# Kernel tuning notes

Hardware: AMD Instinct MI355X
Metric: run time of the kernel (lower is better)

The kernel has to match this reference:

```python
import jax, jax.numpy as jnp
import numpy as np

NUM_KP = 34
NUM_CP = 10
DEGREE = 3
NUM_KNOTS = NUM_CP + DEGREE + 1  # 14
B = 32768


def _lin(k, i, o):
    return jax.random.normal(k, (i, o), jnp.float32) * (1.0 / np.sqrt(i))


def setup_inputs() -> dict:
    key = jax.random.key(0)
    ks = jax.random.split(key, 18)
    keypoints = jax.random.normal(ks[0], (B, NUM_KP, 2), jnp.float32)
    # clamped cubic base knot vector: [0]*4 + 6 interior + [1]*4
    interior = jnp.linspace(0.0, 1.0, 8)[1:-1]
    base = jnp.concatenate([jnp.zeros(4), interior, jnp.ones(4)]).astype(jnp.float32)
    knots = jnp.tile(base[None, :], (B, 1))
    cp = jax.random.normal(ks[1], (B, NUM_CP, 2), jnp.float32)
    return {
        'keypoints': keypoints, 'knots': knots, 'cp': cp,
        'w1': _lin(ks[2], NUM_KP * 2, 256), 'b1': jnp.zeros(256, jnp.float32),
        'w2': _lin(ks[3], 256, 512), 'b2': jnp.zeros(512, jnp.float32),
        'w3': _lin(ks[4], 512, 256), 'b3': jnp.zeros(256, jnp.float32),
        'wc1': _lin(ks[5], 256, 128), 'bc1': jnp.zeros(128, jnp.float32),
        'wc2': _lin(ks[6], 128, NUM_CP * 2), 'bc2': jnp.zeros(NUM_CP * 2, jnp.float32),
        'wk1': _lin(ks[7], 256, 128), 'bk1': jnp.zeros(128, jnp.float32),
        'wk2': _lin(ks[8], 128, NUM_KNOTS - 8), 'bk2': jnp.zeros(NUM_KNOTS - 8, jnp.float32),
    }


def bspline_points(u, cpts, uq):
    """Cox-de Boor evaluation. u: (14,), cpts: (10,2), uq: (Q,). Returns (Q,2)."""
    uq = jnp.minimum(uq, u[-1] - 1e-6)  # handle u=1 endpoint of clamped knots
    # degree-0 basis: (Q, 13)
    N = ((uq[:, None] >= u[None, :-1]) & (uq[:, None] < u[None, 1:])).astype(cpts.dtype)
    for p in range(1, DEGREE + 1):
        left_den = u[p:-1] - u[:-p - 1]
        right_den = u[p + 1:] - u[1:-p]
        left = jnp.where(left_den > 0, (uq[:, None] - u[None, :-p - 1]) / left_den, 0.0)
        right = jnp.where(right_den > 0, (u[None, p + 1:] - uq[:, None]) / right_den, 0.0)
        N = left * N[:, :-1] + right * N[:, 1:]
    return N @ cpts  # (Q,10)@(10,2)


def cobb_line(pts):
    """Cobb angles (PT, MT, TL) in degrees from curve points (34,2)."""
    d = pts[1:] - pts[:-1]  # (33,2) tangents
    ang = jnp.degrees(jnp.arctan2(d[:, 0], d[:, 1]))  # tilt w.r.t. vertical axis
    i_max = jnp.argmax(ang)
    i_min = jnp.argmin(ang)
    mt = ang[i_max] - ang[i_min]
    lo = jnp.minimum(i_max, i_min)
    hi = jnp.maximum(i_max, i_min)
    idx = jnp.arange(ang.shape[0])
    up = jnp.where(idx <= lo, ang, ang[lo])
    pt = jnp.max(up) - jnp.min(up)
    dn = jnp.where(idx >= hi, ang, ang[hi])
    tl = jnp.max(dn) - jnp.min(dn)
    return jnp.stack([pt, mt, tl])


def reference(keypoints, knots, cp, w1, b1, w2, b2, w3, b3,
              wc1, bc1, wc2, bc2, wk1, bk1, wk2, bk2):
    bsz = keypoints.shape[0]
    x = keypoints.reshape(bsz, -1)  # [B, 68]
    # feature extractor (eval mode: dropout = identity)
    h = jax.nn.relu(x @ w1 + b1)
    h = jax.nn.relu(h @ w2 + b2)
    feat = jax.nn.relu(h @ w3 + b3)  # [B, 256]
    # control-point head
    cp_flat = jax.nn.relu(feat @ wc1 + bc1) @ wc2 + bc2
    deta_cp = cp_flat.reshape(bsz, NUM_CP, 2)
    cps = deta_cp + cp
    # knot head with Hardtanh(0,1)
    deta_knots_6 = jnp.clip(jax.nn.relu(feat @ wk1 + bk1) @ wk2 + bk2, 0.0, 1.0)
    zeros4 = jnp.zeros((bsz, 4), deta_knots_6.dtype)
    knots_full = jnp.concatenate([zeros4, deta_knots_6, zeros4], axis=1) + knots
    # batched de-Boor spline eval + Cobb geometry (replaces per-sample loop)
    uq = jnp.linspace(0.0, 1.0, NUM_KP).astype(jnp.float32)
    pts = jax.vmap(lambda u, c: bspline_points(u, c, uq))(knots_full, cps)  # [B,34,2]
    cobb_angles = jax.vmap(cobb_line)(pts)  # [B,3]
    return cobb_angles, deta_cp, deta_knots_6
```

## Files before the change

### kernel.cpp

```cpp
#include <hip/hip_runtime.h>
#include <math.h>

#define BLOCK 256
#define MS 16


__device__ __forceinline__ void unpack16(const float* __restrict__ row, float* av){
  const float4* r4 = (const float4*)row;
  float4 a0=r4[0], a1=r4[1], a2=r4[2], a3=r4[3];
  av[0]=a0.x;  av[1]=a0.y;  av[2]=a0.z;  av[3]=a0.w;
  av[4]=a1.x;  av[5]=a1.y;  av[6]=a1.z;  av[7]=a1.w;
  av[8]=a2.x;  av[9]=a2.y;  av[10]=a2.z; av[11]=a2.w;
  av[12]=a3.x; av[13]=a3.y; av[14]=a3.z; av[15]=a3.w;
}

template<int K, int N, int VEC, bool RELU>
__device__ __forceinline__ void dense_layer(const float* __restrict__ W,
                                            const float* __restrict__ Bv,
                                            const float* sA, float* sC, int tid)
{
  static_assert(N == BLOCK*VEC, "each thread owns VEC consecutive columns");
  const int j0 = tid*VEC;
  float acc[VEC][MS];
  #pragma unroll
  for (int c=0;c<VEC;c++){
    float b = Bv[j0+c];
    #pragma unroll
    for (int m=0;m<MS;m++) acc[c][m] = b;
  }
  #pragma unroll 4
  for (int k=0;k<K;k++){
    float av[MS];
    unpack16(sA + k*MS, av);
    float w[VEC];
    if constexpr (VEC == 2){
      float2 wv = *(const float2*)(W + (size_t)k*N + j0);
      w[0]=wv.x; w[1]=wv.y;
    } else {
      w[0] = W[(size_t)k*N + j0];
    }
    #pragma unroll
    for (int c=0;c<VEC;c++){
      #pragma unroll
      for (int m=0;m<MS;m++) acc[c][m] = fmaf(av[m], w[c], acc[c][m]);
    }
  }
  #pragma unroll
  for (int c=0;c<VEC;c++){
    #pragma unroll
    for (int m=0;m<MS;m++){
      float v = acc[c][m];
      if (RELU) v = fmaxf(v, 0.f);
      sC[(size_t)(j0+c)*MS + m] = v;
    }
  }
}

extern "C" __global__ __launch_bounds__(BLOCK, 3)
void kbs_mlp(const float* __restrict__ kp,
             const float* __restrict__ w1, const float* __restrict__ b1,
             const float* __restrict__ w2, const float* __restrict__ b2,
             const float* __restrict__ w3, const float* __restrict__ b3,
             const float* __restrict__ wc1, const float* __restrict__ bc1,
             const float* __restrict__ wc2, const float* __restrict__ bc2,
             const float* __restrict__ wk1, const float* __restrict__ bk1,
             const float* __restrict__ wk2, const float* __restrict__ bk2,
             float* __restrict__ dout, int B)
{
  __shared__ float sA[512*MS];
  __shared__ float sB[256*MS];

  const int tid = threadIdx.x;
  const long base = (long)blockIdx.x * MS;

  for (int idx = tid; idx < 68*MS; idx += BLOCK){
    int m = idx / 68, k = idx % 68;
    float v = 0.f;
    if (base + m < B) v = kp[(base + m)*68 + k];
    sA[k*MS + m] = v;
  }
  __syncthreads();

  dense_layer<68, 256, 1, true>(w1, b1, sA, sB, tid);
  __syncthreads();
  dense_layer<256,512, 2, true>(w2, b2, sB, sA, tid);
  __syncthreads();
  dense_layer<512,256, 1, true>(w3, b3, sA, sB, tid);
  __syncthreads();

  float* sHC = sA;
  float* sHK = sA + 128*MS;
  {
    const bool isC = (tid < 128);
    const int j = tid & 127;
    const float* W  = isC ? wc1 : wk1;
    const float* Bv = isC ? bc1 : bk1;
    float acc[MS];
    float b = Bv[j];
    #pragma unroll
    for (int m=0;m<MS;m++) acc[m] = b;
    #pragma unroll 4
    for (int k=0;k<256;k++){
      float av[MS];
      unpack16(sB + k*MS, av);
      float w = W[k*128 + j];
      #pragma unroll
      for (int m=0;m<MS;m++) acc[m] = fmaf(av[m], w, acc[m]);
    }
    float* dst = isC ? sHC : sHK;
    #pragma unroll
    for (int m=0;m<MS;m++) dst[j*MS + m] = fmaxf(acc[m], 0.f);
  }
  __syncthreads();

  float* sCPF = sB;
  float* sK6  = sB + 20*MS;
  if (tid < 20){
    float acc[MS];
    float b = bc2[tid];
    #pragma unroll
    for (int m=0;m<MS;m++) acc[m] = b;
    for (int k=0;k<128;k++){
      float av[MS];
      unpack16(sHC + k*MS, av);
      float w = wc2[k*20 + tid];
      #pragma unroll
      for (int m=0;m<MS;m++) acc[m] = fmaf(av[m], w, acc[m]);
    }
    #pragma unroll
    for (int m=0;m<MS;m++) sCPF[tid*MS + m] = acc[m];
  } else if (tid >= 64 && tid < 70){
    const int j = tid - 64;
    float acc[MS];
    float b = bk2[j];
    #pragma unroll
    for (int m=0;m<MS;m++) acc[m] = b;
    for (int k=0;k<128;k++){
      float av[MS];
      unpack16(sHK + k*MS, av);
      float w = wk2[k*6 + j];
      #pragma unroll
      for (int m=0;m<MS;m++) acc[m] = fmaf(av[m], w, acc[m]);
    }
    #pragma unroll
    for (int m=0;m<MS;m++) sK6[j*MS + m] = fminf(fmaxf(acc[m], 0.f), 1.f);
  }
  __syncthreads();

  float* out_dcp = dout + (long)B*3;
  float* out_dk  = dout + (long)B*23;
  for (int idx = tid; idx < MS*20; idx += BLOCK){
    int s = idx / 20, c = idx % 20;
    if (base + s < B) out_dcp[(base+s)*20 + c] = sCPF[c*MS + s];
  }
  for (int idx = tid; idx < MS*6; idx += BLOCK){
    int s = idx / 6, c = idx % 6;
    if (base + s < B) out_dk[(base+s)*6 + c] = sK6[c*MS + s];
  }
}

extern "C" __global__ __launch_bounds__(256)
void kbs_geom(const float* __restrict__ knots_g, const float* __restrict__ cp_g,
              float* __restrict__ dout, int B)
{
  const int s = blockIdx.x * blockDim.x + threadIdx.x;
  if (s >= B) return;

  const float* dcp = dout + (long)B*3  + (long)s*20;
  const float* dk6 = dout + (long)B*23 + (long)s*6;

  double u[14];
  #pragma unroll
  for (int i=0;i<14;i++){
    double d = (i>=4 && i<10) ? (double)dk6[i-4] : 0.0;
    u[i] = (double)knots_g[(long)s*14 + i] + d;
  }
  double cx[10], cy[10];
  #pragma unroll
  for (int i=0;i<10;i++){
    cx[i] = (double)cp_g[(long)s*20 + 2*i    ] + (double)dcp[2*i    ];
    cy[i] = (double)cp_g[(long)s*20 + 2*i + 1] + (double)dcp[2*i + 1];
  }

  double ang[33];
  double ppx = 0.0, ppy = 0.0;
  const double uend = u[13] - 1e-6;
  for (int q = 0; q < 34; ++q){
    double uq = (double)q * (1.0/33.0);
    if (uq > uend) uq = uend;
    double Nb[13];
    #pragma unroll
    for (int i=0;i<13;i++)
      Nb[i] = (uq >= u[i] && uq < u[i+1]) ? 1.0 : 0.0;
    #pragma unroll
    for (int p=1;p<=3;p++){
      #pragma unroll
      for (int i=0;i+p<13;i++){
        double ld = u[i+p]   - u[i];
        double rd = u[i+p+1] - u[i+1];
        double lf = (ld > 0.0) ? (uq - u[i])     / ld : 0.0;
        double rf = (rd > 0.0) ? (u[i+p+1] - uq) / rd : 0.0;
        Nb[i] = lf*Nb[i] + rf*Nb[i+1];
      }
    }
    double px = 0.0, py = 0.0;
    #pragma unroll
    for (int i=0;i<10;i++){ px += Nb[i]*cx[i]; py += Nb[i]*cy[i]; }
    if (q > 0)
      ang[q-1] = 57.29577951308232087679815 * atan2(px - ppx, py - ppy);
    ppx = px; ppy = py;
  }

  int imax = 0, imin = 0;
  for (int i=1;i<33;i++){
    if (ang[i] > ang[imax]) imax = i;
    if (ang[i] < ang[imin]) imin = i;
  }
  double mt = ang[imax] - ang[imin];
  int lo = imax < imin ? imax : imin;
  int hi = imax > imin ? imax : imin;

  double uM = -1e300, um = 1e300;
  for (int i=0;i<=lo;i++){ uM = fmax(uM, ang[i]); um = fmin(um, ang[i]); }
  double dM = -1e300, dm = 1e300;
  for (int i=hi;i<33;i++){ dM = fmax(dM, ang[i]); dm = fmin(dm, ang[i]); }

  dout[(long)s*3 + 0] = (float)(uM - um);
  dout[(long)s*3 + 1] = (float)mt;
  dout[(long)s*3 + 2] = (float)(dM - dm);
}

extern "C" void kernel_launch(void* const* d_in, const int* in_sizes, int n_in,
                              void* d_out, int out_size, void* d_ws, size_t ws_size,
                              hipStream_t stream)
{
  const float* kp    = (const float*)d_in[0];
  const float* knots = (const float*)d_in[1];
  const float* cp    = (const float*)d_in[2];
  const float* w1  = (const float*)d_in[3];  const float* b1  = (const float*)d_in[4];
  const float* w2  = (const float*)d_in[5];  const float* b2  = (const float*)d_in[6];
  const float* w3  = (const float*)d_in[7];  const float* b3  = (const float*)d_in[8];
  const float* wc1 = (const float*)d_in[9];  const float* bc1 = (const float*)d_in[10];
  const float* wc2 = (const float*)d_in[11]; const float* bc2 = (const float*)d_in[12];
  const float* wk1 = (const float*)d_in[13]; const float* bk1 = (const float*)d_in[14];
  const float* wk2 = (const float*)d_in[15]; const float* bk2 = (const float*)d_in[16];

  const int B = in_sizes[0] / 68;
  const int nblkA = (B + MS - 1) / MS;
  const int nblkB = (B + 255) / 256;

  hipLaunchKernelGGL(kbs_mlp, dim3(nblkA), dim3(BLOCK), 0, stream,
                     kp, w1, b1, w2, b2, w3, b3,
                     wc1, bc1, wc2, bc2, wk1, bk1, wk2, bk2,
                     (float*)d_out, B);
  hipLaunchKernelGGL(kbs_geom, dim3(nblkB), dim3(256), 0, stream,
                     knots, cp, (float*)d_out, B);
}
```

Measured before the change: 529.8 us.

## Retile MLP dense layers to 2-4 columns by 8 samples per thread; unroll geometry kernel

```diff
diff --git a/kernel.cpp b/kernel.cpp
--- a/kernel.cpp
+++ b/kernel.cpp
@@ -5,55 +5,45 @@
 #define MS 16
 
 
-__device__ __forceinline__ void unpack16(const float* __restrict__ row, float* av){
-  const float4* r4 = (const float4*)row;
-  float4 a0=r4[0], a1=r4[1], a2=r4[2], a3=r4[3];
-  av[0]=a0.x;  av[1]=a0.y;  av[2]=a0.z;  av[3]=a0.w;
-  av[4]=a1.x;  av[5]=a1.y;  av[6]=a1.z;  av[7]=a1.w;
-  av[8]=a2.x;  av[9]=a2.y;  av[10]=a2.z; av[11]=a2.w;
-  av[12]=a3.x; av[13]=a3.y; av[14]=a3.z; av[15]=a3.w;
-}
-
-template<int K, int N, int VEC, bool RELU>
-__device__ __forceinline__ void dense_layer(const float* __restrict__ W,
-                                            const float* __restrict__ Bv,
-                                            const float* sA, float* sC, int tid)
-{
-  static_assert(N == BLOCK*VEC, "each thread owns VEC consecutive columns");
-  const int j0 = tid*VEC;
-  float acc[VEC][MS];
-  #pragma unroll
-  for (int c=0;c<VEC;c++){
-    float b = Bv[j0+c];
-    #pragma unroll
-    for (int m=0;m<MS;m++) acc[c][m] = b;
+template<int K, int CPT, bool RELU>
+__device__ __forceinline__ void dense_cols(const float* __restrict__ Wcol, int ld,
+                                           const float* __restrict__ Bcol,
+                                           const float* sArow,
+                                           float* sCcol)
+{
+  float acc[CPT][8];
+  #pragma unroll
+  for (int c=0;c<CPT;c++){
+    float b = Bcol[c];
+    #pragma unroll
+    for (int m=0;m<8;m++) acc[c][m] = b;
   }
   #pragma unroll 4
   for (int k=0;k<K;k++){
-    float av[MS];
-    unpack16(sA + k*MS, av);
-    float w[VEC];
-    if constexpr (VEC == 2){
-      float2 wv = *(const float2*)(W + (size_t)k*N + j0);
+    float4 a0 = *(const float4*)(sArow + k*MS);
+    float4 a1 = *(const float4*)(sArow + k*MS + 4);
+    float av[8] = {a0.x,a0.y,a0.z,a0.w,a1.x,a1.y,a1.z,a1.w};
+    float w[CPT];
+    if constexpr (CPT == 4){
+      float4 wv = *(const float4*)(Wcol + (size_t)k*ld);
+      w[0]=wv.x; w[1]=wv.y; w[2]=wv.z; w[3]=wv.w;
+    } else {
+      float2 wv = *(const float2*)(Wcol + (size_t)k*ld);
       w[0]=wv.x; w[1]=wv.y;
-    } else {
-      w[0] = W[(size_t)k*N + j0];
-    }
-    #pragma unroll
-    for (int c=0;c<VEC;c++){
-      #pragma unroll
-      for (int m=0;m<MS;m++) acc[c][m] = fmaf(av[m], w[c], acc[c][m]);
-    }
-  }
-  #pragma unroll
-  for (int c=0;c<VEC;c++){
-    #pragma unroll
-    for (int m=0;m<MS;m++){
+    }
+    #pragma unroll
+    for (int c=0;c<CPT;c++)
+      #pragma unroll
+      for (int m=0;m<8;m++) acc[c][m] = fmaf(av[m], w[c], acc[c][m]);
+  }
+  #pragma unroll
+  for (int c=0;c<CPT;c++)
+    #pragma unroll
+    for (int m=0;m<8;m++){
       float v = acc[c][m];
       if (RELU) v = fmaxf(v, 0.f);
-      sC[(size_t)(j0+c)*MS + m] = v;
-    }
-  }
+      sCcol[c*MS + m] = v;
+    }
 }
 
 extern "C" __global__ __launch_bounds__(BLOCK, 3)
@@ -71,6 +61,8 @@
   __shared__ float sB[256*MS];
 
   const int tid = threadIdx.x;
+  const int j   = tid & 127;
+  const int h   = tid >> 7;
   const long base = (long)blockIdx.x * MS;
 
   for (int idx = tid; idx < 68*MS; idx += BLOCK){
@@ -81,35 +73,17 @@
   }
   __syncthreads();
 
-  dense_layer<68, 256, 1, true>(w1, b1, sA, sB, tid);
-  __syncthreads();
-  dense_layer<256,512, 2, true>(w2, b2, sB, sA, tid);
-  __syncthreads();
-  dense_layer<512,256, 1, true>(w3, b3, sA, sB, tid);
-  __syncthreads();
-
-  float* sHC = sA;
-  float* sHK = sA + 128*MS;
+  dense_cols<68, 2, true>(w1 + 2*j, 256, b1 + 2*j, sA + h*8, sB + (2*j)*MS + h*8);
+  __syncthreads();
+  dense_cols<256, 4, true>(w2 + 4*j, 512, b2 + 4*j, sB + h*8, sA + (4*j)*MS + h*8);
+  __syncthreads();
+  dense_cols<512, 2, true>(w3 + 2*j, 256, b3 + 2*j, sA + h*8, sB + (2*j)*MS + h*8);
+  __syncthreads();
   {
-    const bool isC = (tid < 128);
-    const int j = tid & 127;
-    const float* W  = isC ? wc1 : wk1;
-    const float* Bv = isC ? bc1 : bk1;
-    float acc[MS];
-    float b = Bv[j];
-    #pragma unroll
-    for (int m=0;m<MS;m++) acc[m] = b;
-    #pragma unroll 4
-    for (int k=0;k<256;k++){
-      float av[MS];
-      unpack16(sB + k*MS, av);
-      float w = W[k*128 + j];
-      #pragma unroll
-      for (int m=0;m<MS;m++) acc[m] = fmaf(av[m], w, acc[m]);
-    }
-    float* dst = isC ? sHC : sHK;
-    #pragma unroll
-    for (int m=0;m<MS;m++) dst[j*MS + m] = fmaxf(acc[m], 0.f);
+    const int c0 = 2*j;
+    const float* Wp = (c0 < 128) ? (wc1 + c0) : (wk1 + (c0 - 128));
+    const float* Bp = (c0 < 128) ? (bc1 + c0) : (bk1 + (c0 - 128));
+    dense_cols<256, 2, true>(Wp, 128, Bp, sB + h*8, sA + c0*MS + h*8);
   }
   __syncthreads();
 
@@ -121,8 +95,10 @@
     #pragma unroll
     for (int m=0;m<MS;m++) acc[m] = b;
     for (int k=0;k<128;k++){
-      float av[MS];
-      unpack16(sHC + k*MS, av);
+      const float4* r4 = (const float4*)(sA + k*MS);
+      float4 q0=r4[0], q1=r4[1], q2=r4[2], q3=r4[3];
+      float av[MS] = {q0.x,q0.y,q0.z,q0.w,q1.x,q1.y,q1.z,q1.w,
+                      q2.x,q2.y,q2.z,q2.w,q3.x,q3.y,q3.z,q3.w};
       float w = wc2[k*20 + tid];
       #pragma unroll
       for (int m=0;m<MS;m++) acc[m] = fmaf(av[m], w, acc[m]);
@@ -130,20 +106,22 @@
     #pragma unroll
     for (int m=0;m<MS;m++) sCPF[tid*MS + m] = acc[m];
   } else if (tid >= 64 && tid < 70){
-    const int j = tid - 64;
+    const int jj = tid - 64;
     float acc[MS];
-    float b = bk2[j];
+    float b = bk2[jj];
     #pragma unroll
     for (int m=0;m<MS;m++) acc[m] = b;
     for (int k=0;k<128;k++){
-      float av[MS];
-      unpack16(sHK + k*MS, av);
-      float w = wk2[k*6 + j];
+      const float4* r4 = (const float4*)(sA + (128+k)*MS);
+      float4 q0=r4[0], q1=r4[1], q2=r4[2], q3=r4[3];
+      float av[MS] = {q0.x,q0.y,q0.z,q0.w,q1.x,q1.y,q1.z,q1.w,
+                      q2.x,q2.y,q2.z,q2.w,q3.x,q3.y,q3.z,q3.w};
+      float w = wk2[k*6 + jj];
       #pragma unroll
       for (int m=0;m<MS;m++) acc[m] = fmaf(av[m], w, acc[m]);
     }
     #pragma unroll
-    for (int m=0;m<MS;m++) sK6[j*MS + m] = fminf(fmaxf(acc[m], 0.f), 1.f);
+    for (int m=0;m<MS;m++) sK6[jj*MS + m] = fminf(fmaxf(acc[m], 0.f), 1.f);
   }
   __syncthreads();
 
@@ -159,11 +137,11 @@
   }
 }
 
-extern "C" __global__ __launch_bounds__(256)
+extern "C" __global__ __launch_bounds__(64, 1)
 void kbs_geom(const float* __restrict__ knots_g, const float* __restrict__ cp_g,
               float* __restrict__ dout, int B)
 {
-  const int s = blockIdx.x * blockDim.x + threadIdx.x;
+  const int s = blockIdx.x * 64 + threadIdx.x;
   if (s >= B) return;
 
   const float* dcp = dout + (long)B*3  + (long)s*20;
@@ -185,6 +163,7 @@
   double ang[33];
   double ppx = 0.0, ppy = 0.0;
   const double uend = u[13] - 1e-6;
+  #pragma unroll
   for (int q = 0; q < 34; ++q){
     double uq = (double)q * (1.0/33.0);
     if (uq > uend) uq = uend;
@@ -211,19 +190,23 @@
     ppx = px; ppy = py;
   }
 
+  double vmax = ang[0], vmin = ang[0];
   int imax = 0, imin = 0;
+  #pragma unroll
   for (int i=1;i<33;i++){
-    if (ang[i] > ang[imax]) imax = i;
-    if (ang[i] < ang[imin]) imin = i;
-  }
-  double mt = ang[imax] - ang[imin];
+    if (ang[i] > vmax){ vmax = ang[i]; imax = i; }
+    if (ang[i] < vmin){ vmin = ang[i]; imin = i; }
+  }
+  double mt = vmax - vmin;
   int lo = imax < imin ? imax : imin;
   int hi = imax > imin ? imax : imin;
 
-  double uM = -1e300, um = 1e300;
-  for (int i=0;i<=lo;i++){ uM = fmax(uM, ang[i]); um = fmin(um, ang[i]); }
-  double dM = -1e300, dm = 1e300;
-  for (int i=hi;i<33;i++){ dM = fmax(dM, ang[i]); dm = fmin(dm, ang[i]); }
+  double uM = -1e300, um = 1e300, dM = -1e300, dm = 1e300;
+  #pragma unroll
+  for (int i=0;i<33;i++){
+    if (i <= lo){ uM = fmax(uM, ang[i]); um = fmin(um, ang[i]); }
+    if (i >= hi){ dM = fmax(dM, ang[i]); dm = fmin(dm, ang[i]); }
+  }
 
   dout[(long)s*3 + 0] = (float)(uM - um);
   dout[(long)s*3 + 1] = (float)mt;
@@ -247,12 +230,12 @@
 
   const int B = in_sizes[0] / 68;
   const int nblkA = (B + MS - 1) / MS;
-  const int nblkB = (B + 255) / 256;
+  const int nblkB = (B + 63) / 64;
 
   hipLaunchKernelGGL(kbs_mlp, dim3(nblkA), dim3(BLOCK), 0, stream,
                      kp, w1, b1, w2, b2, w3, b3,
                      wc1, bc1, wc2, bc2, wk1, bk1, wk2, bk2,
                      (float*)d_out, B);
-  hipLaunchKernelGGL(kbs_geom, dim3(nblkB), dim3(256), 0, stream,
+  hipLaunchKernelGGL(kbs_geom, dim3(nblkB), dim3(64), 0, stream,
                      knots, cp, (float*)d_out, B);
 }
```

Measured after the change: 520.7 us. About the same (-1.7%).
